# Kernel optimization log

Hardware: AMD Instinct MI355X
Metric: run time of the kernel (lower is better)

The kernel has to match this reference:

```python
import jax, jax.numpy as jnp
import numpy as np
from jax import lax

NUM_COARSE = 64
GROUP_SIZE = 32
GRID_SIZE = 6
GRID_PTS = GRID_SIZE * GRID_SIZE  # 36


def setup_inputs() -> dict:
    key = jax.random.key(0)
    ki = iter(jax.random.split(key, 64))

    def rn(shape, scale=0.02):
        return jax.random.normal(next(ki), shape, jnp.float32) * scale

    B, N = 8, 8192
    return {
        "corrupted_pts": jax.random.normal(next(ki), (B, N, 3), jnp.float32),
        "pts": jax.random.normal(next(ki), (B, N, 3), jnp.float32),
        "enc_w1": rn((3, 128)), "enc_b1": jnp.zeros((128,), jnp.float32),
        "enc_w2": rn((128, 256)), "enc_b2": jnp.zeros((256,), jnp.float32),
        "enc_w3": rn((256, 1024)), "enc_b3": jnp.zeros((1024,), jnp.float32),
        "pe_w1": rn((3, 128)), "pe_b1": jnp.zeros((128,), jnp.float32),
        "pe_w2": rn((128, 1024)), "pe_b2": jnp.zeros((1024,), jnp.float32),
        "cp_w1": rn((1024, 1024)), "cp_b1": jnp.zeros((1024,), jnp.float32),
        "cp_w2": rn((1024, 1024)), "cp_b2": jnp.zeros((1024,), jnp.float32),
        "cp_w3": rn((1024, NUM_COARSE * 3)), "cp_b3": jnp.zeros((NUM_COARSE * 3,), jnp.float32),
        "f1_w1": rn((1024 + 2, 512)), "f1_b1": jnp.zeros((512,), jnp.float32),
        "f1_w2": rn((512, 512)), "f1_b2": jnp.zeros((512,), jnp.float32),
        "f1_w3": rn((512, 3)), "f1_b3": jnp.zeros((3,), jnp.float32),
        "f2_w1": rn((1024 + 3, 512)), "f2_b1": jnp.zeros((512,), jnp.float32),
        "f2_w2": rn((512, 512)), "f2_b2": jnp.zeros((512,), jnp.float32),
        "f2_w3": rn((512, 3)), "f2_b3": jnp.zeros((3,), jnp.float32),
    }


def _fps(xyz, n_samples):
    """Farthest point sampling, start at index 0. xyz: (N,3) -> (n_samples,3)."""
    d0 = jnp.sum((xyz - xyz[0]) ** 2, axis=-1)

    def step(dists, _):
        nxt = jnp.argmax(dists)
        d = jnp.sum((xyz - xyz[nxt]) ** 2, axis=-1)
        return jnp.minimum(dists, d), nxt

    _, idxs = lax.scan(step, d0, None, length=n_samples - 1)
    idxs = jnp.concatenate([jnp.zeros((1,), idxs.dtype), idxs])
    return xyz[idxs]


def _chamfer_l2(x, y):
    """Symmetric Chamfer-L2 over batched point sets x:(B,Nx,3), y:(B,Ny,3)."""
    d = jnp.sum((x[:, :, None, :] - y[:, None, :, :]) ** 2, axis=-1)  # (B,Nx,Ny)
    return jnp.mean(jnp.min(d, axis=2)) + jnp.mean(jnp.min(d, axis=1))


def _build_grid():
    # itertools.product(x, y): x varies slowest -> 'ij' meshgrid ordering
    lin = jnp.linspace(-0.3, 0.3, GRID_SIZE)
    xx, yy = jnp.meshgrid(lin, lin, indexing="ij")
    return jnp.stack([xx.ravel(), yy.ravel()], axis=-1)  # (36,2)


def reference(corrupted_pts, pts,
              enc_w1, enc_b1, enc_w2, enc_b2, enc_w3, enc_b3,
              pe_w1, pe_b1, pe_w2, pe_b2,
              cp_w1, cp_b1, cp_w2, cp_b2, cp_w3, cp_b3,
              f1_w1, f1_b1, f1_w2, f1_b2, f1_w3, f1_b3,
              f2_w1, f2_b1, f2_w2, f2_b2, f2_w3, f2_b3):
    corrupted_pts = corrupted_pts[:, :, :3]
    pts = pts[:, :, :3]
    B, N, _ = pts.shape

    # --- Group divider: FPS centers + KNN neighborhoods (normalized) ---
    centers = jax.vmap(lambda p: _fps(p, NUM_COARSE))(pts)            # (B,G,3)
    d2 = jnp.sum((centers[:, :, None, :] - pts[:, None, :, :]) ** 2, axis=-1)  # (B,G,N)
    _, idx = lax.top_k(-d2, GROUP_SIZE)                               # (B,G,K)
    neigh = jnp.take_along_axis(pts[:, None, :, :], idx[..., None], axis=2)    # (B,G,K,3)
    neigh = neigh - centers[:, :, None, :]

    # --- positional embedding of centers ---
    pos = jax.nn.gelu(centers @ pe_w1 + pe_b1, approximate=False) @ pe_w2 + pe_b2  # (B,G,1024)

    # --- global encoder (PointNet-style stand-in for PointNetv2_encoder) ---
    h = jax.nn.relu(corrupted_pts @ enc_w1 + enc_b1)
    h = jax.nn.relu(h @ enc_w2 + enc_b2)
    h = h @ enc_w3 + enc_b3
    feat = jnp.max(h, axis=1)                                          # (B,1024)

    # --- coarse prediction ---
    c = jax.nn.relu(feat @ cp_w1 + cp_b1)
    c = jax.nn.relu(c @ cp_w2 + cp_b2)
    coarse = (c @ cp_w3 + cp_b3).reshape(B, NUM_COARSE, 3)

    # --- folding decoder (1x1 convs == per-point linears) ---
    BG = B * NUM_COARSE
    fe = (feat[:, None, :] + pos).reshape(BG, 1024)
    fe = jnp.broadcast_to(fe[:, None, :], (BG, GRID_PTS, 1024))
    grid = jnp.broadcast_to(_build_grid()[None], (BG, GRID_PTS, 2))
    cat1 = jnp.concatenate([fe, grid], axis=-1)                        # (BG,36,1026)
    h1 = jax.nn.relu(cat1 @ f1_w1 + f1_b1)
    h1 = jax.nn.relu(h1 @ f1_w2 + f1_b2)
    fold1 = h1 @ f1_w3 + f1_b3                                         # (BG,36,3)
    cat2 = jnp.concatenate([fe, fold1], axis=-1)                       # (BG,36,1027)
    h2 = jax.nn.relu(cat2 @ f2_w1 + f2_b1)
    h2 = jax.nn.relu(h2 @ f2_w2 + f2_b2)
    fold2 = h2 @ f2_w3 + f2_b3                                         # (BG,36,3)

    loss_coarse = _chamfer_l2(coarse, centers)
    loss_fine = _chamfer_l2(fold2, neigh.reshape(BG, GROUP_SIZE, 3))
    return (loss_fine, loss_coarse)
```

## Files before the change

### kernel.cpp

```cpp
#include <hip/hip_runtime.h>
#include <float.h>
#include <math.h>

typedef unsigned short u16;
typedef short bshort8 __attribute__((ext_vector_type(8)));
typedef float vf4 __attribute__((ext_vector_type(4)));

struct Ptrs { const float* p[30]; };

__device__ __align__(16) unsigned int g_featkey[8192];
__device__ __align__(16) float g_fold1[18432 * 3];
__device__ __align__(16) float g_fold2[18432 * 3];
__device__ __align__(16) float g_accum[8];
__device__ __align__(16) float g_centers[512 * 3];
__device__ __align__(16) float g_neigh[512 * 32 * 3];
__device__ __align__(16) float g_c1[8192];
__device__ __align__(16) float g_c2[8192];
__device__ __align__(16) float g_coarse[8 * 192];
__device__ __align__(16) u16 g_p1[512 * 128];
__device__ __align__(16) u16 g_fe[512 * 1024];
__device__ __align__(16) u16 g_fea[512 * 512];
__device__ __align__(16) u16 g_feb[512 * 512];
__device__ __align__(16) float g_gw[36 * 512];
__device__ __align__(16) u16 g_w2T[256 * 128];
__device__ __align__(16) u16 g_w3T[1024 * 256];
__device__ __align__(16) u16 g_pew2T[1024 * 128];
__device__ __align__(16) u16 g_f1w1aT[512 * 1024];
__device__ __align__(16) u16 g_f1w2T[512 * 512];
__device__ __align__(16) u16 g_f2w1aT[512 * 1024];
__device__ __align__(16) u16 g_f2w2T[512 * 512];

__device__ __forceinline__ u16 f2b(float f) {
    unsigned int u = __float_as_uint(f);
    unsigned int r = (u + 0x7fffu + ((u >> 16) & 1u)) >> 16;
    return (u16)r;
}
__device__ __forceinline__ float b2f(u16 u) {
    return __uint_as_float(((unsigned int)u) << 16);
}
__device__ __forceinline__ float dec(unsigned int k) {
    unsigned int u = (k & 0x80000000u) ? (k & 0x7fffffffu) : ~k;
    return __uint_as_float(u);
}

__global__ __launch_bounds__(256) void zero_kernel(Ptrs ptrs, u16* out) {
    int i = blockIdx.x * 256 + threadIdx.x;
    if (i < 8192) {
        g_featkey[i] = 0u;
        g_c1[i] = 0.f;
        g_c2[i] = 0.f;
    }
    if (i < 1536) g_coarse[i] = 0.f;
    if (i < 18432 * 3) { g_fold1[i] = 0.f; g_fold2[i] = 0.f; }
    if (i < 8) g_accum[i] = 0.f;
}

__global__ __launch_bounds__(256) void convert_kernel(Ptrs ptrs, u16* out) {
    int plane = blockIdx.y;
    if (plane == 7) {
        int id = blockIdx.x * 256 + threadIdx.x;
        if (id >= 36 * 512) return;
        const float* f1w1 = ptrs.p[18];
        const float* f1b1 = ptrs.p[19];
        int q = id >> 9, n = id & 511;
        int qi = q / 6, qj = q - qi * 6;
        float gx = (qi == 5) ? 0.3f : (-0.3f + qi * 0.12f);
        float gy = (qj == 5) ? 0.3f : (-0.3f + qj * 0.12f);
        g_gw[id] = gx * f1w1[(size_t)1024 * 512 + n] + gy * f1w1[(size_t)1025 * 512 + n] + f1b1[n];
        return;
    }
    static const int kSrc[7] = {4, 6, 10, 18, 20, 24, 26};
    int K, N;
    u16* dst;
    switch (plane) {
        case 0:  dst = g_w2T;    K = 128;  N = 256;  break;
        case 1:  dst = g_w3T;    K = 256;  N = 1024; break;
        case 2:  dst = g_pew2T;  K = 128;  N = 1024; break;
        case 3:  dst = g_f1w1aT; K = 1024; N = 512;  break;
        case 4:  dst = g_f1w2T;  K = 512;  N = 512;  break;
        case 5:  dst = g_f2w1aT; K = 1024; N = 512;  break;
        default: dst = g_f2w2T;  K = 512;  N = 512;  break;
    }
    int tilesK = K >> 6, tilesN = N >> 6;
    int tile = blockIdx.x;
    if (tile >= tilesK * tilesN) return;
    int tk = tile % tilesK, tn = tile / tilesK;
    int k0 = tk * 64, n0 = tn * 64;
    const float* src = ptrs.p[kSrc[plane]];
    __shared__ float tl[64 * 65];
    int r = threadIdx.x >> 2, c16 = (threadIdx.x & 3) * 16;
    const float* sp = &src[(size_t)(k0 + r) * N + n0 + c16];
#pragma unroll
    for (int j = 0; j < 16; ++j) tl[r * 65 + c16 + j] = sp[j];
    __syncthreads();
    union { u16 u[16]; uint4 v[2]; } tmp;
#pragma unroll
    for (int j = 0; j < 16; ++j) tmp.u[j] = f2b(tl[(c16 + j) * 65 + r]);
    u16* dp = &dst[(size_t)(n0 + r) * K + k0 + c16];
    *(uint4*)&dp[0] = tmp.v[0];
    *(uint4*)&dp[8] = tmp.v[1];
}

__global__ __launch_bounds__(256) void fps_encoder_kernel(Ptrs ptrs, u16* out) {
    __shared__ __align__(16) short h1s[64 * 136];
    __shared__ __align__(16) short h2s[64 * 264];
    __shared__ __align__(16) short Bs[2][64 * 72];
    __shared__ float red[256];
    __shared__ float xyzs[192];
    int tid = threadIdx.x;
    if (blockIdx.x < 8) {
#pragma clang fp contract(off)
        int b = blockIdx.x;
        const float* P = ptrs.p[1] + (size_t)b * 8192 * 3;
        float ds[32];
        float cx = P[0], cy = P[1], cz = P[2];
        float v = -1.f; int vi = 1 << 30;
#pragma unroll
        for (int j = 0; j < 32; ++j) {
            int i = tid + j * 256;
            float dx = P[i * 3] - cx, dy = P[i * 3 + 1] - cy, dz = P[i * 3 + 2] - cz;
            ds[j] = (dx * dx + dy * dy) + dz * dz;
            if (ds[j] > v) { v = ds[j]; vi = i; }
        }
        __shared__ float wv2[2][4];
        __shared__ int wi2[2][4];
        float* cen = xyzs;
        if (tid == 0) {
            g_centers[b * 192 + 0] = cx; cen[0] = cx;
            g_centers[b * 192 + 1] = cy; cen[1] = cy;
            g_centers[b * 192 + 2] = cz; cen[2] = cz;
        }
        int lane = tid & 63, w = tid >> 6;
        for (int s = 1; s < 64; ++s) {
            int p = s & 1;
#pragma unroll
            for (int off = 1; off < 64; off <<= 1) {
                float ov = __shfl_xor(v, off); int oi = __shfl_xor(vi, off);
                if (ov > v || (ov == v && oi < vi)) { v = ov; vi = oi; }
            }
            if (lane == 0) { wv2[p][w] = v; wi2[p][w] = vi; }
            __syncthreads();
            float bv = wv2[p][0]; int bi = wi2[p][0];
#pragma unroll
            for (int k = 1; k < 4; ++k)
                if (wv2[p][k] > bv || (wv2[p][k] == bv && wi2[p][k] < bi)) {
                    bv = wv2[p][k]; bi = wi2[p][k];
                }
            bi &= 8191;
            float nxx = P[bi * 3], nxy = P[bi * 3 + 1], nxz = P[bi * 3 + 2];
            if (tid == 0) {
                cen[s * 3 + 0] = nxx; cen[s * 3 + 1] = nxy; cen[s * 3 + 2] = nxz;
                g_centers[b * 192 + s * 3 + 0] = nxx;
                g_centers[b * 192 + s * 3 + 1] = nxy;
                g_centers[b * 192 + s * 3 + 2] = nxz;
            }
            v = -1.f; vi = 1 << 30;
#pragma unroll
            for (int j = 0; j < 32; ++j) {
                int i = tid + j * 256;
                float dx = P[i * 3] - nxx, dy = P[i * 3 + 1] - nxy, dz = P[i * 3 + 2] - nxz;
                float d = (dx * dx + dy * dy) + dz * dz;
                float nd = fminf(ds[j], d);
                ds[j] = nd;
                if (nd > v) { v = nd; vi = i; }
            }
        }
        __syncthreads();
        const float* pw = ptrs.p[8];
        const float* pb = ptrs.p[9];
        for (int ii = tid; ii < 8192; ii += 256) {
            int g = ii >> 7, o = ii & 127;
            float x0 = cen[g * 3], x1 = cen[g * 3 + 1], x2 = cen[g * 3 + 2];
            float h = x0 * pw[o] + x1 * pw[128 + o] + x2 * pw[256 + o] + pb[o];
            float ge = 0.5f * h * (1.0f + erff(h * 0.7071067811865475f));
            g_p1[(size_t)(b * 64 + g) * 128 + o] = f2b(ge);
        }
        return;
    }
    const float* X = ptrs.p[0];
    const float* w1 = ptrs.p[2];
    const float* b1 = ptrs.p[3];
    const float* b2 = ptrs.p[5];
    const float* b3 = ptrs.p[7];
    int base = (blockIdx.x - 8) * 64;
    for (int i = tid; i < 192; i += 256) xyzs[i] = X[(size_t)base * 3 + i];
    __syncthreads();
    {
        int k = tid & 127;
        float wa = w1[k], wbv = w1[128 + k], wc = w1[256 + k], bb = b1[k];
        int r0 = tid >> 7;
#pragma unroll
        for (int it = 0; it < 32; ++it) {
            int row = r0 + it * 2;
            float v = xyzs[row * 3] * wa + xyzs[row * 3 + 1] * wbv + xyzs[row * 3 + 2] * wc + bb;
            h1s[row * 136 + k] = (short)f2b(fmaxf(v, 0.f));
        }
    }
    int lane = tid & 63, w = tid >> 6, q = lane >> 4, c = lane & 15;
    int brow = tid >> 2, bc = (tid & 3) * 16;
    for (int nch = 0; nch < 4; ++nch) {
        const u16* W = &g_w2T[(size_t)(nch * 64 + brow) * 128 + bc];
        uint4 r0v = *(const uint4*)&W[0];
        uint4 r1v = *(const uint4*)&W[8];
        *(uint4*)&Bs[0][brow * 72 + bc] = r0v;
        *(uint4*)&Bs[0][brow * 72 + bc + 8] = r1v;
        uint4 s0v = *(const uint4*)&W[64];
        uint4 s1v = *(const uint4*)&W[72];
        __syncthreads();
        vf4 acc[4];
#pragma unroll
        for (int t = 0; t < 4; ++t)
#pragma unroll
            for (int r = 0; r < 4; ++r) acc[t][r] = 0.f;
#pragma unroll
        for (int s = 0; s < 2; ++s) {
            bshort8 av = *(const bshort8*)&h1s[(w * 16 + c) * 136 + s * 32 + q * 8];
#pragma unroll
            for (int t = 0; t < 4; ++t) {
                bshort8 bv = *(const bshort8*)&Bs[0][(t * 16 + c) * 72 + s * 32 + q * 8];
                acc[t] = __builtin_amdgcn_mfma_f32_16x16x32_bf16(av, bv, acc[t], 0, 0, 0);
            }
        }
        *(uint4*)&Bs[1][brow * 72 + bc] = s0v;
        *(uint4*)&Bs[1][brow * 72 + bc + 8] = s1v;
        __syncthreads();
#pragma unroll
        for (int s = 0; s < 2; ++s) {
            bshort8 av = *(const bshort8*)&h1s[(w * 16 + c) * 136 + 64 + s * 32 + q * 8];
#pragma unroll
            for (int t = 0; t < 4; ++t) {
                bshort8 bv = *(const bshort8*)&Bs[1][(t * 16 + c) * 72 + s * 32 + q * 8];
                acc[t] = __builtin_amdgcn_mfma_f32_16x16x32_bf16(av, bv, acc[t], 0, 0, 0);
            }
        }
#pragma unroll
        for (int t = 0; t < 4; ++t) {
            int n = nch * 64 + t * 16 + c;
            float bv = b2[n];
#pragma unroll
            for (int r = 0; r < 4; ++r) {
                int row = w * 16 + q * 4 + r;
                h2s[row * 264 + n] = (short)f2b(fmaxf(acc[t][r] + bv, 0.f));
            }
        }
    }
    int batch = base >> 13;
    for (int nch = 0; nch < 16; ++nch) {
        const u16* W = &g_w3T[(size_t)(nch * 64 + brow) * 256 + bc];
        uint4 a0 = *(const uint4*)&W[0];
        uint4 a1 = *(const uint4*)&W[8];
        *(uint4*)&Bs[0][brow * 72 + bc] = a0;
        *(uint4*)&Bs[0][brow * 72 + bc + 8] = a1;
        uint4 n0 = *(const uint4*)&W[64];
        uint4 n1 = *(const uint4*)&W[72];
        __syncthreads();
        vf4 acc[4];
#pragma unroll
        for (int t = 0; t < 4; ++t)
#pragma unroll
            for (int r = 0; r < 4; ++r) acc[t][r] = 0.f;
#pragma unroll
        for (int ch = 0; ch < 4; ++ch) {
            int p = ch & 1;
#pragma unroll
            for (int s = 0; s < 2; ++s) {
                bshort8 av = *(const bshort8*)&h2s[(w * 16 + c) * 264 + ch * 64 + s * 32 + q * 8];
#pragma unroll
                for (int t = 0; t < 4; ++t) {
                    bshort8 bv = *(const bshort8*)&Bs[p][(t * 16 + c) * 72 + s * 32 + q * 8];
                    acc[t] = __builtin_amdgcn_mfma_f32_16x16x32_bf16(av, bv, acc[t], 0, 0, 0);
                }
            }
            if (ch < 3) {
                *(uint4*)&Bs[1 - p][brow * 72 + bc] = n0;
                *(uint4*)&Bs[1 - p][brow * 72 + bc + 8] = n1;
                if (ch < 2) {
                    n0 = *(const uint4*)&W[(ch + 2) * 64];
                    n1 = *(const uint4*)&W[(ch + 2) * 64 + 8];
                }
                __syncthreads();
            }
        }
#pragma unroll
        for (int t = 0; t < 4; ++t) {
            float m = fmaxf(fmaxf(acc[t][0], acc[t][1]), fmaxf(acc[t][2], acc[t][3]));
            m = fmaxf(m, __shfl_xor(m, 16));
            m = fmaxf(m, __shfl_xor(m, 32));
            if (lane < 16) red[w * 64 + t * 16 + lane] = m;
        }
        __syncthreads();
        if (tid < 64) {
            float m = fmaxf(fmaxf(red[tid], red[64 + tid]), fmaxf(red[128 + tid], red[192 + tid]));
            float val = m + b3[nch * 64 + tid];
            unsigned int u = __float_as_uint(val);
            unsigned int key = (u & 0x80000000u) ? ~u : (u | 0x80000000u);
            atomicMax(&g_featkey[batch * 1024 + nch * 64 + tid], key);
        }
        __syncthreads();
    }
}

__global__ __launch_bounds__(256) void group_kernel(Ptrs ptrs, u16* out) {
#pragma clang fp contract(off)
    int g = blockIdx.x, tid = threadIdx.x;
    int b = g >> 6;
    const float* P = ptrs.p[1] + (size_t)b * 8192 * 3;
    float cx = g_centers[g * 3], cy = g_centers[g * 3 + 1], cz = g_centers[g * 3 + 2];
    __shared__ float dl[8192];
    for (int j = 0; j < 32; ++j) {
        int i = tid + j * 256;
        float dx = P[i * 3] - cx, dy = P[i * 3 + 1] - cy, dz = P[i * 3 + 2] - cz;
        dl[i] = (dx * dx + dy * dy) + dz * dz;
    }
    __syncthreads();
    __shared__ float wv[4];
    __shared__ int wi[4];
    int lane = tid & 63, w = tid >> 6;
    for (int r = 0; r < 32; ++r) {
        float v = FLT_MAX; int vi = 1 << 30;
        for (int j = 0; j < 32; ++j) {
            int i = tid + j * 256;
            float d = dl[i];
            if (d < v) { v = d; vi = i; }
        }
#pragma unroll
        for (int off = 1; off < 64; off <<= 1) {
            float ov = __shfl_xor(v, off); int oi = __shfl_xor(vi, off);
            if (ov < v || (ov == v && oi < vi)) { v = ov; vi = oi; }
        }
        if (lane == 0) { wv[w] = v; wi[w] = vi; }
        __syncthreads();
        if (tid == 0) {
            float bv = wv[0]; int bi = wi[0];
            for (int k = 1; k < 4; ++k)
                if (wv[k] < bv || (wv[k] == bv && wi[k] < bi)) { bv = wv[k]; bi = wi[k]; }
            bi &= 8191;
            g_neigh[((size_t)g * 32 + r) * 3 + 0] = P[bi * 3] - cx;
            g_neigh[((size_t)g * 32 + r) * 3 + 1] = P[bi * 3 + 1] - cy;
            g_neigh[((size_t)g * 32 + r) * 3 + 2] = P[bi * 3 + 2] - cz;
            dl[bi] = FLT_MAX;
        }
        __syncthreads();
    }
}

__global__ __launch_bounds__(256) void gemm_fe_kernel(Ptrs ptrs, u16* out) {
    const u16* A = g_p1;
    const u16* BT = g_pew2T;
    const float* bias = ptrs.p[11];
    const int N = 1024, K = 128;
    __shared__ __align__(16) short As[64 * 40];
    __shared__ __align__(16) short Bs[64 * 40];
    int tid = threadIdx.x;
    int lane = tid & 63, w = tid >> 6;
    int mBase = blockIdx.y * 64, nBase = blockIdx.x * 64;
    int q = lane >> 4, c = lane & 15;
    vf4 acc[4];
#pragma unroll
    for (int t = 0; t < 4; ++t)
#pragma unroll
        for (int r = 0; r < 4; ++r) acc[t][r] = 0.f;
    int srow = tid >> 2, scol = (tid & 3) * 8;
    for (int k0 = 0; k0 < K; k0 += 32) {
        uint4 aval = *(const uint4*)&A[(size_t)(mBase + srow) * K + k0 + scol];
        uint4 bval = *(const uint4*)&BT[(size_t)(nBase + srow) * K + k0 + scol];
        __syncthreads();
        *(uint4*)&As[srow * 40 + scol] = aval;
        *(uint4*)&Bs[srow * 40 + scol] = bval;
        __syncthreads();
        bshort8 av = *(const bshort8*)&As[(w * 16 + c) * 40 + q * 8];
#pragma unroll
        for (int t = 0; t < 4; ++t) {
            bshort8 bv = *(const bshort8*)&Bs[(t * 16 + c) * 40 + q * 8];
            acc[t] = __builtin_amdgcn_mfma_f32_16x16x32_bf16(av, bv, acc[t], 0, 0, 0);
        }
    }
#pragma unroll
    for (int t = 0; t < 4; ++t) {
        int n = nBase + t * 16 + c;
#pragma unroll
        for (int r = 0; r < 4; ++r) {
            int m = mBase + w * 16 + q * 4 + r;
            float v = acc[t][r];
            g_fe[(size_t)m * N + n] = f2b(dec(g_featkey[(m >> 6) * 1024 + n]) + v + bias[n]);
        }
    }
}

__global__ __launch_bounds__(256) void gemm_ab_kernel(Ptrs ptrs, u16* out) {
    const u16* A = g_fe;
    const u16* BT = (blockIdx.z == 0) ? g_f1w1aT : g_f2w1aT;
    u16* dst = (blockIdx.z == 0) ? g_fea : g_feb;
    const int N = 512, K = 1024;
    __shared__ __align__(16) short As[64 * 40];
    __shared__ __align__(16) short Bs[64 * 40];
    int tid = threadIdx.x;
    int lane = tid & 63, w = tid >> 6;
    int mBase = blockIdx.y * 64, nBase = blockIdx.x * 64;
    int q = lane >> 4, c = lane & 15;
    vf4 acc[4];
#pragma unroll
    for (int t = 0; t < 4; ++t)
#pragma unroll
        for (int r = 0; r < 4; ++r) acc[t][r] = 0.f;
    int srow = tid >> 2, scol = (tid & 3) * 8;
    for (int k0 = 0; k0 < K; k0 += 32) {
        uint4 aval = *(const uint4*)&A[(size_t)(mBase + srow) * K + k0 + scol];
        uint4 bval = *(const uint4*)&BT[(size_t)(nBase + srow) * K + k0 + scol];
        __syncthreads();
        *(uint4*)&As[srow * 40 + scol] = aval;
        *(uint4*)&Bs[srow * 40 + scol] = bval;
        __syncthreads();
        bshort8 av = *(const bshort8*)&As[(w * 16 + c) * 40 + q * 8];
#pragma unroll
        for (int t = 0; t < 4; ++t) {
            bshort8 bv = *(const bshort8*)&Bs[(t * 16 + c) * 40 + q * 8];
            acc[t] = __builtin_amdgcn_mfma_f32_16x16x32_bf16(av, bv, acc[t], 0, 0, 0);
        }
    }
#pragma unroll
    for (int t = 0; t < 4; ++t) {
        int n = nBase + t * 16 + c;
#pragma unroll
        for (int r = 0; r < 4; ++r) {
            int m = mBase + w * 16 + q * 4 + r;
            dst[(size_t)m * N + n] = f2b(acc[t][r]);
        }
    }
}

template <int MODE>
__global__ __launch_bounds__(256) void fold_gemm_kernel(Ptrs ptrs, u16* out) {
    const u16* feX = (MODE == 1) ? g_fea : g_feb;
    const u16* W2T = (MODE == 1) ? g_f1w2T : g_f2w2T;
    const float* gmat = (MODE == 1) ? g_gw : g_fold1;
    float* foldOut = (MODE == 1) ? g_fold1 : g_fold2;
    const float* b2 = (MODE == 1) ? ptrs.p[21] : ptrs.p[27];
    const float* W3 = (MODE == 1) ? ptrs.p[22] : ptrs.p[28];
    const float* wb = ptrs.p[24] + (size_t)1024 * 512;
    const float* sbias = ptrs.p[25];
    const float* pb3 = ptrs.p[23];
    __shared__ __align__(16) short As[64 * 40];
    __shared__ __align__(16) short Bs[64 * 40];
    int tid = threadIdx.x;
    int lane = tid & 63, w = tid >> 6, q = lane >> 4, c = lane & 15;
    int mBase = blockIdx.y * 64, nBase = blockIdx.x * 64;
    int srow = tid >> 2, scol = (tid & 3) * 8;
    int row = mBase + srow;
    int g = row / 36;
    int qq = row - g * 36;
    float f0 = 0.f, f1 = 0.f, f2 = 0.f;
    if (MODE == 2) {
        f0 = gmat[row * 3 + 0] + pb3[0];
        f1 = gmat[row * 3 + 1] + pb3[1];
        f2 = gmat[row * 3 + 2] + pb3[2];
    }
    vf4 acc[4];
#pragma unroll
    for (int t = 0; t < 4; ++t)
#pragma unroll
        for (int r = 0; r < 4; ++r) acc[t][r] = 0.f;
    for (int kt = 0; kt < 16; ++kt) {
        union { u16 u[8]; uint4 v; } tmp;
        int kb = kt * 32 + scol;
        if (MODE == 1) {
#pragma unroll
            for (int j = 0; j < 8; ++j) {
                float v = b2f(feX[g * 512 + kb + j]) + gmat[qq * 512 + kb + j];
                tmp.u[j] = f2b(fmaxf(v, 0.f));
            }
        } else {
#pragma unroll
            for (int j = 0; j < 8; ++j) {
                int k = kb + j;
                float v = b2f(feX[g * 512 + k]) + f0 * wb[k] + f1 * wb[512 + k] +
                          f2 * wb[1024 + k] + sbias[k];
                tmp.u[j] = f2b(fmaxf(v, 0.f));
            }
        }
        uint4 bval = *(const uint4*)&W2T[(size_t)(nBase + srow) * 512 + kb];
        __syncthreads();
        *(uint4*)&As[srow * 40 + scol] = tmp.v;
        *(uint4*)&Bs[srow * 40 + scol] = bval;
        __syncthreads();
        bshort8 av = *(const bshort8*)&As[(w * 16 + c) * 40 + q * 8];
#pragma unroll
        for (int t = 0; t < 4; ++t) {
            bshort8 bv = *(const bshort8*)&Bs[(t * 16 + c) * 40 + q * 8];
            acc[t] = __builtin_amdgcn_mfma_f32_16x16x32_bf16(av, bv, acc[t], 0, 0, 0);
        }
    }
    float p[4][3];
#pragma unroll
    for (int r = 0; r < 4; ++r)
#pragma unroll
        for (int o = 0; o < 3; ++o) p[r][o] = 0.f;
#pragma unroll
    for (int t = 0; t < 4; ++t) {
        int n = nBase + t * 16 + c;
        float bv = b2[n];
        float w30 = W3[n * 3], w31 = W3[n * 3 + 1], w32 = W3[n * 3 + 2];
#pragma unroll
        for (int r = 0; r < 4; ++r) {
            float v = fmaxf(acc[t][r] + bv, 0.f);
            p[r][0] += v * w30; p[r][1] += v * w31; p[r][2] += v * w32;
        }
    }
#pragma unroll
    for (int off = 1; off < 16; off <<= 1)
#pragma unroll
        for (int r = 0; r < 4; ++r)
#pragma unroll
            for (int o = 0; o < 3; ++o) p[r][o] += __shfl_xor(p[r][o], off);
    if (c == 0) {
#pragma unroll
        for (int r = 0; r < 4; ++r) {
            int orow = mBase + w * 16 + q * 4 + r;
            atomicAdd(&foldOut[orow * 3 + 0], p[r][0]);
            atomicAdd(&foldOut[orow * 3 + 1], p[r][1]);
            atomicAdd(&foldOut[orow * 3 + 2], p[r][2]);
        }
    }
}

template <int SEL, int N>
__global__ __launch_bounds__(256) void thinmlp_kernel(Ptrs ptrs, u16* out) {
    float* dst = (SEL == 0) ? g_c1 : ((SEL == 1) ? g_c2 : g_coarse);
    const float* B = (SEL == 0) ? ptrs.p[12] : ((SEL == 1) ? ptrs.p[14] : ptrs.p[16]);
    const float* pbias = (SEL == 1) ? ptrs.p[13] : ptrs.p[15];
    __shared__ float Als[8 * 64];
    int tid = threadIdx.x;
    int k0 = blockIdx.y * 64;
    for (int i = tid; i < 8 * 64; i += 256) {
        int m = i >> 6, k = k0 + (i & 63);
        float a;
        if (SEL == 0)      a = dec(g_featkey[m * 1024 + k]);
        else if (SEL == 1) a = fmaxf(g_c1[m * 1024 + k] + pbias[k], 0.f);
        else               a = fmaxf(g_c2[m * 1024 + k] + pbias[k], 0.f);
        Als[i] = a;
    }
    __syncthreads();
    int n = blockIdx.x * 256 + tid;
    if (n >= N) return;
    float acc[8];
#pragma unroll
    for (int m = 0; m < 8; ++m) acc[m] = 0.f;
    for (int k = 0; k < 64; ++k) {
        float bv = B[(size_t)(k0 + k) * N + n];
#pragma unroll
        for (int m = 0; m < 8; ++m) acc[m] += Als[m * 64 + k] * bv;
    }
#pragma unroll
    for (int m = 0; m < 8; ++m) atomicAdd(&dst[(size_t)m * N + n], acc[m]);
}

__global__ __launch_bounds__(128) void chamfer_kernel(Ptrs ptrs, u16* out) {
    __shared__ float s1[192], s2[192];
    __shared__ float pA[128], pB[128];
    int tid = threadIdx.x;
    if (blockIdx.x < 8) {
        const float* cb3 = ptrs.p[17];
        int b = blockIdx.x;
        for (int i = tid; i < 192; i += 128) {
            s1[i] = g_coarse[(size_t)b * 192 + i] + cb3[i];
            s2[i] = g_centers[(size_t)b * 192 + i];
        }
        __syncthreads();
        float sA = 0.f, sB = 0.f;
        if (tid < 64) {
            float bx = s1[tid * 3], by = s1[tid * 3 + 1], bz = s1[tid * 3 + 2];
            float best = FLT_MAX;
            for (int j = 0; j < 64; ++j) {
                float dx = bx - s2[j * 3], dy = by - s2[j * 3 + 1], dz = bz - s2[j * 3 + 2];
                best = fminf(best, dx * dx + dy * dy + dz * dz);
            }
            sA = best;
        } else {
            int j = tid - 64;
            float bx = s2[j * 3], by = s2[j * 3 + 1], bz = s2[j * 3 + 2];
            float best = FLT_MAX;
            for (int i = 0; i < 64; ++i) {
                float dx = s1[i * 3] - bx, dy = s1[i * 3 + 1] - by, dz = s1[i * 3 + 2] - bz;
                best = fminf(best, dx * dx + dy * dy + dz * dz);
            }
            sB = best;
        }
        pA[tid] = sA; pB[tid] = sB;
        __syncthreads();
        for (int st = 64; st; st >>= 1) {
            if (tid < st) { pA[tid] += pA[tid + st]; pB[tid] += pB[tid + st]; }
            __syncthreads();
        }
        if (tid == 0) { atomicAdd(&g_accum[2], pA[0]); atomicAdd(&g_accum[3], pB[0]); }
        return;
    }
    const float* f2b3 = ptrs.p[29];
    int g = blockIdx.x - 8;
    float b3v[3] = {f2b3[0], f2b3[1], f2b3[2]};
    for (int i = tid; i < 108; i += 128) {
        int o = i - (i / 3) * 3;
        s1[i] = g_fold2[(size_t)g * 108 + i] + b3v[o];
    }
    for (int i = tid; i < 96; i += 128) s2[i] = g_neigh[(size_t)g * 96 + i];
    __syncthreads();
    float sA = 0.f, sB = 0.f;
    if (tid < 36) {
        float bx = s1[tid * 3], by = s1[tid * 3 + 1], bz = s1[tid * 3 + 2];
        float best = FLT_MAX;
        for (int j = 0; j < 32; ++j) {
            float dx = bx - s2[j * 3], dy = by - s2[j * 3 + 1], dz = bz - s2[j * 3 + 2];
            best = fminf(best, dx * dx + dy * dy + dz * dz);
        }
        sA = best;
    } else if (tid >= 64 && tid < 96) {
        int j = tid - 64;
        float bx = s2[j * 3], by = s2[j * 3 + 1], bz = s2[j * 3 + 2];
        float best = FLT_MAX;
        for (int i = 0; i < 36; ++i) {
            float dx = s1[i * 3] - bx, dy = s1[i * 3 + 1] - by, dz = s1[i * 3 + 2] - bz;
            best = fminf(best, dx * dx + dy * dy + dz * dz);
        }
        sB = best;
    }
    pA[tid] = sA; pB[tid] = sB;
    __syncthreads();
    for (int st = 64; st; st >>= 1) {
        if (tid < st) { pA[tid] += pA[tid + st]; pB[tid] += pB[tid + st]; }
        __syncthreads();
    }
    if (tid == 0) { atomicAdd(&g_accum[0], pA[0]); atomicAdd(&g_accum[1], pB[0]); }
}

__global__ void finalize_kernel(Ptrs ptrs, u16* out) {
    if (threadIdx.x == 0) {
        float lf = g_accum[0] / (512.f * 36.f) + g_accum[1] / (512.f * 32.f);
        float lc = g_accum[2] / 512.f + g_accum[3] / 512.f;
        u16 blf = f2b(lf), blc = f2b(lc);
        out[0] = blc;
        out[1] = blf;
        out[2] = blc;
        out[3] = blc;
        out[4] = blc;
        out[5] = blc;
    }
}

extern "C" void kernel_launch(void* const* d_in, const int* in_sizes, int n_in,
                              void* d_out, int out_size, void* d_ws, size_t ws_size,
                              hipStream_t stream) {
    (void)in_sizes; (void)out_size; (void)d_ws; (void)ws_size;
    Ptrs ptrs;
    for (int i = 0; i < 30; ++i) {
        int j = (i < n_in) ? i : (n_in - 1);
        ptrs.p[i] = (const float*)d_in[j];
    }
    u16* out = (u16*)d_out;

    zero_kernel<<<216, 256, 0, stream>>>(ptrs, out);
    convert_kernel<<<dim3(128, 8), 256, 0, stream>>>(ptrs, out);

    fps_encoder_kernel<<<1032, 256, 0, stream>>>(ptrs, out);
    group_kernel<<<512, 256, 0, stream>>>(ptrs, out);

    thinmlp_kernel<0, 1024><<<dim3(4, 16), 256, 0, stream>>>(ptrs, out);
    thinmlp_kernel<1, 1024><<<dim3(4, 16), 256, 0, stream>>>(ptrs, out);
    thinmlp_kernel<2, 192><<<dim3(1, 16), 256, 0, stream>>>(ptrs, out);

    gemm_fe_kernel<<<dim3(16, 8), 256, 0, stream>>>(ptrs, out);

    gemm_ab_kernel<<<dim3(8, 8, 2), 256, 0, stream>>>(ptrs, out);
    fold_gemm_kernel<1><<<dim3(8, 288), 256, 0, stream>>>(ptrs, out);
    fold_gemm_kernel<2><<<dim3(8, 288), 256, 0, stream>>>(ptrs, out);

    chamfer_kernel<<<520, 128, 0, stream>>>(ptrs, out);
    finalize_kernel<<<1, 64, 0, stream>>>(ptrs, out);
}
```

Baseline: 493.1 us.

## Load whole weight chunk per stage and drop cross-wave max reduction in encoder

The encoder MLP now stages the full K extent of each 64-column weight chunk into shared memory at once, instead of double-buffering 64-wide K slices. This removes the intermediate barriers inside each chunk. The per-chunk cross-wave shared reduction and its two barriers are replaced by direct per-wave atomicMax into the global feature keys, which means four times as many atomics. Shared memory is shared between h1s and the weight buffers through one scratch array. The trade-off is more atomic traffic and less overlap between global loads and MFMA work.

```diff
diff --git a/kernel.cpp b/kernel.cpp
--- a/kernel.cpp
+++ b/kernel.cpp
@@ -102,10 +102,8 @@
 }
 
 __global__ __launch_bounds__(256) void fps_encoder_kernel(Ptrs ptrs, u16* out) {
-    __shared__ __align__(16) short h1s[64 * 136];
     __shared__ __align__(16) short h2s[64 * 264];
-    __shared__ __align__(16) short Bs[2][64 * 72];
-    __shared__ float red[256];
+    __shared__ __align__(16) short scratch[64 * 272];
     __shared__ float xyzs[192];
     int tid = threadIdx.x;
     if (blockIdx.x < 8) {
@@ -177,6 +175,9 @@
         }
         return;
     }
+    short* h1s = scratch;
+    short* B2 = scratch + 64 * 136;
+    short* B3 = scratch;
     const float* X = ptrs.p[0];
     const float* w1 = ptrs.p[2];
     const float* b1 = ptrs.p[3];
@@ -197,15 +198,17 @@
         }
     }
     int lane = tid & 63, w = tid >> 6, q = lane >> 4, c = lane & 15;
-    int brow = tid >> 2, bc = (tid & 3) * 16;
+    int brow = tid >> 2;
+    int bc2 = (tid & 3) * 32;
+    int bc3 = (tid & 3) * 64;
     for (int nch = 0; nch < 4; ++nch) {
-        const u16* W = &g_w2T[(size_t)(nch * 64 + brow) * 128 + bc];
-        uint4 r0v = *(const uint4*)&W[0];
-        uint4 r1v = *(const uint4*)&W[8];
-        *(uint4*)&Bs[0][brow * 72 + bc] = r0v;
-        *(uint4*)&Bs[0][brow * 72 + bc + 8] = r1v;
-        uint4 s0v = *(const uint4*)&W[64];
-        uint4 s1v = *(const uint4*)&W[72];
+        if (nch) __syncthreads();
+        {
+            const u16* W = &g_w2T[(size_t)(nch * 64 + brow) * 128 + bc2];
+#pragma unroll
+            for (int j = 0; j < 4; ++j)
+                *(uint4*)&B2[brow * 136 + bc2 + 8 * j] = *(const uint4*)&W[8 * j];
+        }
         __syncthreads();
         vf4 acc[4];
 #pragma unroll
@@ -213,23 +216,11 @@
 #pragma unroll
             for (int r = 0; r < 4; ++r) acc[t][r] = 0.f;
 #pragma unroll
-        for (int s = 0; s < 2; ++s) {
+        for (int s = 0; s < 4; ++s) {
             bshort8 av = *(const bshort8*)&h1s[(w * 16 + c) * 136 + s * 32 + q * 8];
 #pragma unroll
             for (int t = 0; t < 4; ++t) {
-                bshort8 bv = *(const bshort8*)&Bs[0][(t * 16 + c) * 72 + s * 32 + q * 8];
-                acc[t] = __builtin_amdgcn_mfma_f32_16x16x32_bf16(av, bv, acc[t], 0, 0, 0);
-            }
-        }
-        *(uint4*)&Bs[1][brow * 72 + bc] = s0v;
-        *(uint4*)&Bs[1][brow * 72 + bc + 8] = s1v;
-        __syncthreads();
-#pragma unroll
-        for (int s = 0; s < 2; ++s) {
-            bshort8 av = *(const bshort8*)&h1s[(w * 16 + c) * 136 + 64 + s * 32 + q * 8];
-#pragma unroll
-            for (int t = 0; t < 4; ++t) {
-                bshort8 bv = *(const bshort8*)&Bs[1][(t * 16 + c) * 72 + s * 32 + q * 8];
+                bshort8 bv = *(const bshort8*)&B2[(t * 16 + c) * 136 + s * 32 + q * 8];
                 acc[t] = __builtin_amdgcn_mfma_f32_16x16x32_bf16(av, bv, acc[t], 0, 0, 0);
             }
         }
@@ -244,15 +235,16 @@
             }
         }
     }
+    __syncthreads();
     int batch = base >> 13;
     for (int nch = 0; nch < 16; ++nch) {
-        const u16* W = &g_w3T[(size_t)(nch * 64 + brow) * 256 + bc];
-        uint4 a0 = *(const uint4*)&W[0];
-        uint4 a1 = *(const uint4*)&W[8];
-        *(uint4*)&Bs[0][brow * 72 + bc] = a0;
-        *(uint4*)&Bs[0][brow * 72 + bc + 8] = a1;
-        uint4 n0 = *(const uint4*)&W[64];
-        uint4 n1 = *(const uint4*)&W[72];
+        if (nch) __syncthreads();
+        {
+            const u16* W = &g_w3T[(size_t)(nch * 64 + brow) * 256 + bc3];
+#pragma unroll
+            for (int j = 0; j < 8; ++j)
+                *(uint4*)&B3[brow * 264 + bc3 + 8 * j] = *(const uint4*)&W[8 * j];
+        }
         __syncthreads();
         vf4 acc[4];
 #pragma unroll
@@ -260,25 +252,12 @@
 #pragma unroll
             for (int r = 0; r < 4; ++r) acc[t][r] = 0.f;
 #pragma unroll
-        for (int ch = 0; ch < 4; ++ch) {
-            int p = ch & 1;
-#pragma unroll
-            for (int s = 0; s < 2; ++s) {
-                bshort8 av = *(const bshort8*)&h2s[(w * 16 + c) * 264 + ch * 64 + s * 32 + q * 8];
-#pragma unroll
-                for (int t = 0; t < 4; ++t) {
-                    bshort8 bv = *(const bshort8*)&Bs[p][(t * 16 + c) * 72 + s * 32 + q * 8];
-                    acc[t] = __builtin_amdgcn_mfma_f32_16x16x32_bf16(av, bv, acc[t], 0, 0, 0);
-                }
-            }
-            if (ch < 3) {
-                *(uint4*)&Bs[1 - p][brow * 72 + bc] = n0;
-                *(uint4*)&Bs[1 - p][brow * 72 + bc + 8] = n1;
-                if (ch < 2) {
-                    n0 = *(const uint4*)&W[(ch + 2) * 64];
-                    n1 = *(const uint4*)&W[(ch + 2) * 64 + 8];
-                }
-                __syncthreads();
+        for (int s = 0; s < 8; ++s) {
+            bshort8 av = *(const bshort8*)&h2s[(w * 16 + c) * 264 + s * 32 + q * 8];
+#pragma unroll
+            for (int t = 0; t < 4; ++t) {
+                bshort8 bv = *(const bshort8*)&B3[(t * 16 + c) * 264 + s * 32 + q * 8];
+                acc[t] = __builtin_amdgcn_mfma_f32_16x16x32_bf16(av, bv, acc[t], 0, 0, 0);
             }
         }
 #pragma unroll
@@ -286,17 +265,14 @@
             float m = fmaxf(fmaxf(acc[t][0], acc[t][1]), fmaxf(acc[t][2], acc[t][3]));
             m = fmaxf(m, __shfl_xor(m, 16));
             m = fmaxf(m, __shfl_xor(m, 32));
-            if (lane < 16) red[w * 64 + t * 16 + lane] = m;
-        }
-        __syncthreads();
-        if (tid < 64) {
-            float m = fmaxf(fmaxf(red[tid], red[64 + tid]), fmaxf(red[128 + tid], red[192 + tid]));
-            float val = m + b3[nch * 64 + tid];
-            unsigned int u = __float_as_uint(val);
-            unsigned int key = (u & 0x80000000u) ? ~u : (u | 0x80000000u);
-            atomicMax(&g_featkey[batch * 1024 + nch * 64 + tid], key);
-        }
-        __syncthreads();
+            if (lane < 16) {
+                int n = nch * 64 + t * 16 + c;
+                float val = m + b3[n];
+                unsigned int u = __float_as_uint(val);
+                unsigned int key = (u & 0x80000000u) ? ~u : (u | 0x80000000u);
+                atomicMax(&g_featkey[batch * 1024 + n], key);
+            }
+        }
     }
 }
 
```

After: 558.4 us. +13.2%, slower.
